# Kernel tuning notes

Hardware: AMD Instinct MI355X
Metric: run time of the kernel (lower is better)

Reference implementation:

```python
import jax, jax.numpy as jnp
import numpy as np

V, D, L, H, SLOTS, FF = 32000, 1024, 6, 16, 4096, 4096
DH = D // H

def rmsnorm(x, w, eps=1e-8):
    return x * jax.lax.rsqrt(jnp.mean(x * x, axis=-1, keepdims=True) + eps) * w

def rope(x):
    # x: [B,T,D]; interleaved RoPE over full d_model as in RoPEEmbedding
    T = x.shape[1]
    inv_freq = 1.0 / (10000.0 ** (jnp.arange(0, D, 2, dtype=jnp.float32) / D))
    freqs = jnp.arange(T, dtype=jnp.float32)[:, None] * inv_freq[None, :]  # [T, D/2]
    cos, sin = jnp.cos(freqs), jnp.sin(freqs)
    x1, x2 = x[..., ::2], x[..., 1::2]
    out = jnp.stack([x1 * cos - x2 * sin, x1 * sin + x2 * cos], axis=-1)
    return out.reshape(x.shape)

def block(x, Wq, Wk, Wv, Wo, bo, n1, Wg, Wu, Wd, n2):
    B, T, _ = x.shape
    q = (x @ Wq).reshape(B, T, H, DH)
    k = (x @ Wk).reshape(B, T, H, DH)
    v = (x @ Wv).reshape(B, T, H, DH)
    scores = jnp.einsum('bqhd,bkhd->bhqk', q, k) * (DH ** -0.5)
    attn = jax.nn.softmax(scores, axis=-1)
    o = jnp.einsum('bhqk,bkhd->bqhd', attn, v).reshape(B, T, D)
    x = rmsnorm(x + o @ Wo + bo, n1)
    ff = (jax.nn.silu(x @ Wg) * (x @ Wu)) @ Wd
    return rmsnorm(x + ff, n2)

def setup_inputs() -> dict:
    key = jax.random.key(0)
    ks = jax.random.split(key, 20)
    nrm = lambda k, s: (jax.random.normal(k, s, jnp.float32) * 0.02)
    inp = {
        'ids': jax.random.randint(ks[0], (2, 2048), 0, V),
        'tok_embed': nrm(ks[1], (V, D)),
        'Wq': nrm(ks[2], (L, D, D)), 'Wk': nrm(ks[3], (L, D, D)),
        'Wv': nrm(ks[4], (L, D, D)), 'Wo': nrm(ks[5], (L, D, D)),
        'bo': jnp.zeros((L, D), jnp.float32),
        'n1': jnp.ones((L, D), jnp.float32),
        'Wg': nrm(ks[6], (L, D, FF)), 'Wu': nrm(ks[7], (L, D, FF)),
        'Wd': nrm(ks[8], (L, FF, D)),
        'n2': jnp.ones((L, D), jnp.float32),
        'mem': nrm(ks[9], (SLOTS, D)),
        'Wsp': nrm(ks[10], (D, D)), 'bsp': jnp.zeros((D,), jnp.float32),
        'Wrp': nrm(ks[11], (D, D)), 'brp': jnp.zeros((D,), jnp.float32),
        'nout': jnp.ones((D,), jnp.float32),
    }
    return inp

def reference(ids, tok_embed, Wq, Wk, Wv, Wo, bo, n1, Wg, Wu, Wd, n2,
              mem, Wsp, bsp, Wrp, brp, nout):
    x = tok_embed[ids]            # [B,T,D] gather
    x = rope(x)
    for i in range(L):
        x = block(x, Wq[i], Wk[i], Wv[i], Wo[i], bo[i], n1[i],
                  Wg[i], Wu[i], Wd[i], n2[i])
    # StateBank content-addressed read: route queries over memory slots
    q = x @ Wsp + bsp                                   # [B,T,D]
    slot_scores = jnp.einsum('btd,sd->bts', q, mem) * (D ** -0.5)
    attention_maps = jax.nn.softmax(slot_scores, axis=-1)  # [B,T,SLOTS]
    r = jnp.einsum('bts,sd->btd', attention_maps, mem)     # gather-route read
    r = r @ Wrp + brp
    h = rmsnorm(x + r, nout)
    logits = h @ tok_embed.T      # tied lm_head
    return logits
```

## Files before the change

### kernel.cpp

```cpp
#include <hip/hip_runtime.h>

typedef __bf16 bf16;
typedef __attribute__((ext_vector_type(8))) __bf16 bf16x8;
typedef __attribute__((ext_vector_type(4))) __bf16 bf16x4;
typedef __attribute__((ext_vector_type(4))) float f32x4;

#define NL 6
#define DIM 1024
#define NH 16
#define DH 64
#define TT 2048
#define BB 2
#define BT 4096
#define FFD 4096
#define NSLOT 4096
#define NV 32000

__device__ __forceinline__ void gld16(const void* g, void* l) {
  __builtin_amdgcn_global_load_lds(
      (const __attribute__((address_space(1))) void*)g,
      (__attribute__((address_space(3))) void*)l, 16, 0, 0);
}


__global__ void cvt_bf16(const float* __restrict__ s, bf16* __restrict__ d, long n) {
  long i = ((long)blockIdx.x * 256 + threadIdx.x) * 4;
  if (i + 3 < n) {
    float4 v = *(const float4*)(s + i);
    bf16x4 o = {(bf16)v.x, (bf16)v.y, (bf16)v.z, (bf16)v.w};
    *(bf16x4*)(d + i) = o;
  }
}

__global__ void transpose_cvt(const float* __restrict__ src, bf16* __restrict__ dst, int R, int C) {
  __shared__ float tile[32][33];
  int c0 = blockIdx.x * 32, r0 = blockIdx.y * 32;
  int tx = threadIdx.x, ty = threadIdx.y;
#pragma unroll
  for (int i = 0; i < 4; ++i)
    tile[ty + i * 8][tx] = src[(size_t)(r0 + ty + i * 8) * C + c0 + tx];
  __syncthreads();
#pragma unroll
  for (int i = 0; i < 4; ++i)
    dst[(size_t)(c0 + ty + i * 8) * R + r0 + tx] = (bf16)tile[tx][ty + i * 8];
}

__global__ void transpose_v(const bf16* __restrict__ v, int ldv, bf16* __restrict__ vT) {
  __shared__ bf16 tile[32][33];
  int t0 = blockIdx.x * 32, d0 = blockIdx.y * 32, bh = blockIdx.z;
  int b = bh >> 4, h = bh & 15;
  int tx = threadIdx.x, ty = threadIdx.y;
#pragma unroll
  for (int i = 0; i < 4; ++i)
    tile[ty + i * 8][tx] = v[(size_t)(b * TT + t0 + ty + i * 8) * ldv + h * DH + d0 + tx];
  __syncthreads();
#pragma unroll
  for (int i = 0; i < 4; ++i)
    vT[((size_t)bh * DH + d0 + ty + i * 8) * TT + t0 + tx] = tile[tx][ty + i * 8];
}


__global__ void embed_rope(const int* __restrict__ ids, const float* __restrict__ emb,
                           float* __restrict__ xf, bf16* __restrict__ xb) {
  int bt = blockIdx.x;
  int t = bt & (TT - 1);
  int id = ids[bt];
  const float* row = emb + (size_t)id * DIM;
  for (int p = threadIdx.x; p < DIM / 2; p += 256) {
    float x1 = row[2 * p], x2 = row[2 * p + 1];
    float inv = __expf(-9.210340371976184f * (float)p * (1.0f / 512.0f));
    float ang = (float)t * inv;
    float c = cosf(ang), s = sinf(ang);
    float o1 = x1 * c - x2 * s;
    float o2 = x1 * s + x2 * c;
    size_t base = (size_t)bt * DIM + 2 * p;
    xf[base] = o1; xf[base + 1] = o2;
    xb[base] = (bf16)o1; xb[base + 1] = (bf16)o2;
  }
}

enum { EP_BF16 = 0, EP_F32 = 1, EP_F32_BIAS = 2, EP_BF16_BIAS = 3, EP_SILU_MUL = 4 };


template <int EP>
__global__ __launch_bounds__(512, 1) void gemm8(
    const bf16* __restrict__ A, const bf16* __restrict__ Bt, void* __restrict__ Cp,
    const float* __restrict__ bias, const bf16* __restrict__ aux,
    int M, int N, int K) {
  __shared__ bf16 S[4][2][256 * 32];

  const int tid = threadIdx.x;
  const int lane = tid & 63;
  const int r16 = lane & 15, hi = lane >> 4;
  const int wave = tid >> 6;
  const int wm = wave >> 2, wn = wave & 3;

  const int nwg = gridDim.x;
  const int orig = blockIdx.x;
  const int qq = nwg >> 3, rr = nwg & 7;
  const int xcd = orig & 7, cidx = orig >> 3;
  const int wg = (xcd < rr ? xcd * (qq + 1) : rr * (qq + 1) + (xcd - rr) * qq) + cidx;
  const int gM = M / 256;
  const int m0 = (wg % gM) * 256;
  const int n0 = (wg / gM) * 256;

  const int srow = tid >> 2;
  const int ccol = tid & 3;
  const int skey = (srow >> 1) & 3;
  const int gcol = (ccol ^ skey) * 8;
  const bf16* aS = A + (size_t)(m0 + srow) * K + gcol;
  const bf16* bS = Bt + (size_t)(n0 + srow) * K + gcol;
  const int dst0 = tid * 8;

  const int rkey = (r16 >> 1) & 3;
  const int rchunk = (hi ^ rkey) * 8;

  f32x4 acc[8][4] = {};
  const int NT = K / 32;

#pragma unroll
  for (int s = 0; s < 3; ++s) {
    gld16(aS + s * 32, &S[s][0][dst0]);
    gld16(aS + s * 32 + (size_t)128 * K, &S[s][0][dst0 + 4096]);
    gld16(bS + s * 32, &S[s][1][dst0]);
    gld16(bS + s * 32 + (size_t)128 * K, &S[s][1][dst0 + 4096]);
  }
  asm volatile("s_waitcnt vmcnt(8)" ::: "memory");
  __builtin_amdgcn_s_barrier();
  __builtin_amdgcn_sched_barrier(0);

  for (int s = 0; s < NT; ++s) {
    const int cs = s & 3, ps = (s + 3) & 3;
    const bool pre = (s + 3) < NT;
    const bf16* SA = S[cs][0];
    const bf16* SB = S[cs][1];
    const size_t koff = (size_t)(s + 3) * 32;
    bf16x8 af[4], bfr[4];

#pragma unroll
    for (int j = 0; j < 4; ++j)
      bfr[j] = *(const bf16x8*)&SB[(wn * 64 + j * 16 + r16) * 32 + rchunk];
#pragma unroll
    for (int i = 0; i < 4; ++i)
      af[i] = *(const bf16x8*)&SA[(wm * 128 + i * 16 + r16) * 32 + rchunk];
    if (pre) {
      gld16(aS + koff, &S[ps][0][dst0]);
      gld16(aS + koff + (size_t)128 * K, &S[ps][0][dst0 + 4096]);
    }
    __builtin_amdgcn_s_barrier();
    __builtin_amdgcn_sched_barrier(0);
    __builtin_amdgcn_s_setprio(1);
#pragma unroll
    for (int i = 0; i < 4; ++i)
#pragma unroll
      for (int j = 0; j < 4; ++j)
        acc[i][j] = __builtin_amdgcn_mfma_f32_16x16x32_bf16(af[i], bfr[j], acc[i][j], 0, 0, 0);
    __builtin_amdgcn_s_setprio(0);
    __builtin_amdgcn_s_barrier();
    __builtin_amdgcn_sched_barrier(0);

#pragma unroll
    for (int i = 0; i < 4; ++i)
      af[i] = *(const bf16x8*)&SA[(wm * 128 + 64 + i * 16 + r16) * 32 + rchunk];
    if (pre) {
      gld16(bS + koff, &S[ps][1][dst0]);
      gld16(bS + koff + (size_t)128 * K, &S[ps][1][dst0 + 4096]);
    }
    __builtin_amdgcn_s_barrier();
    __builtin_amdgcn_sched_barrier(0);
    __builtin_amdgcn_s_setprio(1);
#pragma unroll
    for (int i = 0; i < 4; ++i)
#pragma unroll
      for (int j = 0; j < 4; ++j)
        acc[4 + i][j] = __builtin_amdgcn_mfma_f32_16x16x32_bf16(af[i], bfr[j], acc[4 + i][j], 0, 0, 0);
    __builtin_amdgcn_s_setprio(0);
    if (pre)               asm volatile("s_waitcnt vmcnt(8)" ::: "memory");
    else if ((s + 2) < NT) asm volatile("s_waitcnt vmcnt(4)" ::: "memory");
    else if ((s + 1) < NT) asm volatile("s_waitcnt vmcnt(0)" ::: "memory");
    __builtin_amdgcn_s_barrier();
    __builtin_amdgcn_sched_barrier(0);
  }

#pragma unroll
  for (int mi = 0; mi < 8; ++mi) {
    const int m = m0 + wm * 128 + mi * 16 + hi * 4;
#pragma unroll
    for (int j = 0; j < 4; ++j) {
      const int n = n0 + wn * 64 + j * 16 + r16;
#pragma unroll
      for (int q = 0; q < 4; ++q) {
        size_t idx = (size_t)(m + q) * N + n;
        float v = acc[mi][j][q];
        if constexpr (EP == EP_F32) {
          ((float*)Cp)[idx] = v;
        } else if constexpr (EP == EP_F32_BIAS) {
          ((float*)Cp)[idx] = v + bias[n];
        } else if constexpr (EP == EP_BF16) {
          ((bf16*)Cp)[idx] = (bf16)v;
        } else if constexpr (EP == EP_BF16_BIAS) {
          ((bf16*)Cp)[idx] = (bf16)(v + bias[n]);
        } else {
          float sg = v / (1.0f + __expf(-v));
          ((bf16*)Cp)[idx] = (bf16)(sg * (float)aux[idx]);
        }
      }
    }
  }
}


template <int BM, int BN, int WMW, int WNW, int EP>
__global__ __launch_bounds__(WMW * WNW * 64, 2) void gemmk(
    const bf16* __restrict__ A, const bf16* __restrict__ Bt, void* __restrict__ Cp,
    const float* __restrict__ bias, const bf16* __restrict__ aux,
    int M, int N, int K) {
  constexpr int BK = 32;
  constexpr int NWAVE = WMW * WNW;
  constexpr int NTHR = NWAVE * 64;
  constexpr int MF = BM / (WMW * 16);
  constexpr int NF = BN / (WNW * 16);
  constexpr int AE = BM * BK;
  constexpr int BE = BN * BK;
  constexpr int RHALF = NTHR / 4;
  __shared__ bf16 sA[4][AE];
  __shared__ bf16 sB[4][BE];

  const int tid = threadIdx.x;
  const int lane = tid & 63;
  const int r16 = lane & 15, hi = lane >> 4;
  const int wave = tid >> 6;
  const int wm = wave / WNW, wn = wave % WNW;

  const int nwg = gridDim.x;
  const int orig = blockIdx.x;
  const int qq = nwg >> 3, rr = nwg & 7;
  const int xcd = orig & 7, cidx = orig >> 3;
  const int wg = (xcd < rr ? xcd * (qq + 1) : rr * (qq + 1) + (xcd - rr) * qq) + cidx;
  const int gM = M / BM;
  const int m0 = (wg % gM) * BM;
  const int n0 = (wg / gM) * BN;

  const int srow = tid >> 2;
  const int ccol = tid & 3;
  const int skey = (srow >> 1) & 3;
  const int gcol = ((ccol ^ skey)) * 8;
  const bf16* aS = A + (size_t)(m0 + srow) * K + gcol;
  const bf16* bS = Bt + (size_t)(n0 + srow) * K + gcol;
  const int dst0 = srow * BK + ccol * 8;

  const int rkey = (r16 >> 1) & 3;
  const int rchunk = (hi ^ rkey) * 8;

  f32x4 acc[MF][NF] = {};
  const int NT = K / BK;

  gld16(aS, &sA[0][dst0]);
  gld16(aS + (size_t)RHALF * K, &sA[0][dst0 + RHALF * BK]);
  gld16(bS, &sB[0][dst0]);
  gld16(bS + (size_t)RHALF * K, &sB[0][dst0 + RHALF * BK]);
  gld16(aS + BK, &sA[1][dst0]);
  gld16(aS + BK + (size_t)RHALF * K, &sA[1][dst0 + RHALF * BK]);
  gld16(bS + BK, &sB[1][dst0]);
  gld16(bS + BK + (size_t)RHALF * K, &sB[1][dst0 + RHALF * BK]);

  for (int t = 0; t < NT; ++t) {
    const int cb = t & 3;
    const int pb = (t + 2) & 3;
    const bool pre = (t + 2) < NT;
    if (pre) {
      gld16(aS + (size_t)(t + 2) * BK, &sA[pb][dst0]);
      gld16(aS + (size_t)(t + 2) * BK + (size_t)RHALF * K, &sA[pb][dst0 + RHALF * BK]);
    }
    if (pre)             asm volatile("s_waitcnt vmcnt(6)" ::: "memory");
    else if (t + 1 < NT) asm volatile("s_waitcnt vmcnt(4)" ::: "memory");
    else                 asm volatile("s_waitcnt vmcnt(0)" ::: "memory");
    __builtin_amdgcn_s_barrier();
    __builtin_amdgcn_sched_barrier(0);

    bf16x8 bf_[NF];
#pragma unroll
    for (int j = 0; j < NF; ++j)
      bf_[j] = *(const bf16x8*)&sB[cb][(wn * (NF * 16) + j * 16 + r16) * BK + rchunk];
    if (pre) {
      gld16(bS + (size_t)(t + 2) * BK, &sB[pb][dst0]);
      gld16(bS + (size_t)(t + 2) * BK + (size_t)RHALF * K, &sB[pb][dst0 + RHALF * BK]);
    }
    bf16x8 af[MF];
#pragma unroll
    for (int i = 0; i < MF; ++i)
      af[i] = *(const bf16x8*)&sA[cb][(wm * (MF * 16) + i * 16 + r16) * BK + rchunk];
    __builtin_amdgcn_s_setprio(1);
#pragma unroll
    for (int i = 0; i < MF; ++i)
#pragma unroll
      for (int j = 0; j < NF; ++j)
        acc[i][j] = __builtin_amdgcn_mfma_f32_16x16x32_bf16(af[i], bf_[j], acc[i][j], 0, 0, 0);
    __builtin_amdgcn_s_setprio(0);
  }

#pragma unroll
  for (int i = 0; i < MF; ++i) {
    const int m = m0 + wm * (MF * 16) + i * 16 + hi * 4;
#pragma unroll
    for (int j = 0; j < NF; ++j) {
      const int n = n0 + wn * (NF * 16) + j * 16 + r16;
#pragma unroll
      for (int q = 0; q < 4; ++q) {
        size_t idx = (size_t)(m + q) * N + n;
        float v = acc[i][j][q];
        if constexpr (EP == EP_F32) {
          ((float*)Cp)[idx] = v;
        } else if constexpr (EP == EP_F32_BIAS) {
          ((float*)Cp)[idx] = v + bias[n];
        } else if constexpr (EP == EP_BF16) {
          ((bf16*)Cp)[idx] = (bf16)v;
        } else if constexpr (EP == EP_BF16_BIAS) {
          ((bf16*)Cp)[idx] = (bf16)(v + bias[n]);
        } else {
          float sg = v / (1.0f + __expf(-v));
          ((bf16*)Cp)[idx] = (bf16)(sg * (float)aux[idx]);
        }
      }
    }
  }
}


__global__ __launch_bounds__(256, 2) void attn_flash(
    const bf16* __restrict__ Qp, const bf16* __restrict__ Kp, int ldk,
    const bf16* __restrict__ Vt, bf16* __restrict__ Op) {
  __shared__ bf16 Ks[2][128 * 32];
  __shared__ bf16 Vs[4][64 * 32];
  __shared__ bf16 Ps[4][4][16 * 40];
  const int tid = threadIdx.x, lane = tid & 63, wave = tid >> 6;
  const int h = blockIdx.y, b = blockIdx.z;
  const int r16 = lane & 15, hi = lane >> 4;
  const int qrow = blockIdx.x * 64 + wave * 16 + r16;

  bf16x8 qa[2];
  {
    const bf16* qp = Qp + (size_t)(b * TT + qrow) * ldk + h * DH + hi * 8;
    qa[0] = *(const bf16x8*)qp;
    qa[1] = *(const bf16x8*)(qp + 32);
  }
  const bf16* kBase = Kp + (size_t)(b * TT) * ldk + h * DH;
  const bf16* vBase = Vt + (size_t)(b * NH + h) * DH * TT;

  const int srow = tid >> 2, ccol = tid & 3;
  const int skey = (srow >> 1) & 3;
  const int scolS = (ccol ^ skey) * 8;
  const int dstc = ccol * 8;
  const int rkey = (r16 >> 1) & 3;
  const int rchunk = (hi ^ rkey) * 8;

  float m_run[4] = {-1e30f, -1e30f, -1e30f, -1e30f};
  float l_run[4] = {0.f, 0.f, 0.f, 0.f};
  f32x4 oacc[4] = {};

  for (int kt = 0; kt < TT; kt += 128) {
#pragma unroll
    for (int half = 0; half < 2; ++half) {
      gld16(kBase + (size_t)(kt + srow) * ldk + half * 32 + scolS, &Ks[half][srow * 32 + dstc]);
      gld16(kBase + (size_t)(kt + 64 + srow) * ldk + half * 32 + scolS, &Ks[half][(64 + srow) * 32 + dstc]);
    }
#pragma unroll
    for (int ks = 0; ks < 4; ++ks)
      gld16(vBase + (size_t)srow * TT + kt + ks * 32 + scolS, &Vs[ks][srow * 32 + dstc]);
    __syncthreads();

    f32x4 s[8];
#pragma unroll
    for (int kg = 0; kg < 8; ++kg) {
      f32x4 z = {};
      bf16x8 kb0 = *(const bf16x8*)&Ks[0][(kg * 16 + r16) * 32 + rchunk];
      bf16x8 kb1 = *(const bf16x8*)&Ks[1][(kg * 16 + r16) * 32 + rchunk];
      z = __builtin_amdgcn_mfma_f32_16x16x32_bf16(qa[0], kb0, z, 0, 0, 0);
      z = __builtin_amdgcn_mfma_f32_16x16x32_bf16(qa[1], kb1, z, 0, 0, 0);
      s[kg] = z * 0.125f;
    }
#pragma unroll
    for (int i = 0; i < 4; ++i) {
      float pm = s[0][i];
#pragma unroll
      for (int kg = 1; kg < 8; ++kg) pm = fmaxf(pm, s[kg][i]);
      pm = fmaxf(pm, __shfl_xor(pm, 1));
      pm = fmaxf(pm, __shfl_xor(pm, 2));
      pm = fmaxf(pm, __shfl_xor(pm, 4));
      pm = fmaxf(pm, __shfl_xor(pm, 8));
      float mnew = fmaxf(m_run[i], pm);
      float sc = __expf(m_run[i] - mnew);
      m_run[i] = mnew;
      l_run[i] *= sc;
#pragma unroll
      for (int n = 0; n < 4; ++n) oacc[n][i] *= sc;
#pragma unroll
      for (int kg = 0; kg < 8; ++kg) {
        float p = __expf(s[kg][i] - mnew);
        l_run[i] += p;
        Ps[wave][kg >> 1][(hi * 4 + i) * 40 + (kg & 1) * 16 + r16] = (bf16)p;
      }
    }
#pragma unroll
    for (int ks = 0; ks < 4; ++ks) {
      bf16x8 pa = *(const bf16x8*)&Ps[wave][ks][r16 * 40 + hi * 8];
#pragma unroll
      for (int n = 0; n < 4; ++n) {
        bf16x8 vb = *(const bf16x8*)&Vs[ks][(n * 16 + r16) * 32 + rchunk];
        oacc[n] = __builtin_amdgcn_mfma_f32_16x16x32_bf16(pa, vb, oacc[n], 0, 0, 0);
      }
    }
    __syncthreads();
  }

#pragma unroll
  for (int i = 0; i < 4; ++i) {
    float l = l_run[i];
    l += __shfl_xor(l, 1);
    l += __shfl_xor(l, 2);
    l += __shfl_xor(l, 4);
    l += __shfl_xor(l, 8);
    float inv = 1.0f / l;
    int trow = blockIdx.x * 64 + wave * 16 + hi * 4 + i;
    size_t base = ((size_t)b * TT + trow) * DIM + h * DH;
#pragma unroll
    for (int n = 0; n < 4; ++n)
      Op[base + n * 16 + r16] = (bf16)(oacc[n][i] * inv);
  }
}


__global__ __launch_bounds__(256) void resid_rms(
    const float* __restrict__ xin, const float* __restrict__ y, const float* __restrict__ wgt,
    float* __restrict__ xf_out, bf16* __restrict__ xb_out) {
  __shared__ float red[4];
  const int r = blockIdx.x, tid = threadIdx.x;
  const size_t base = (size_t)r * DIM + tid * 4;
  float4 v = *(const float4*)(xin + base);
  float4 u = *(const float4*)(y + base);
  v.x += u.x; v.y += u.y; v.z += u.z; v.w += u.w;
  float ss = v.x * v.x + v.y * v.y + v.z * v.z + v.w * v.w;
#pragma unroll
  for (int d = 1; d < 64; d <<= 1) ss += __shfl_xor(ss, d);
  if ((tid & 63) == 0) red[tid >> 6] = ss;
  __syncthreads();
  ss = red[0] + red[1] + red[2] + red[3];
  float sc = rsqrtf(ss * (1.0f / DIM) + 1e-8f);
  const float4 wv = *(const float4*)(wgt + tid * 4);
  float o0 = v.x * sc * wv.x, o1 = v.y * sc * wv.y, o2 = v.z * sc * wv.z, o3 = v.w * sc * wv.w;
  if (xf_out) {
    float4 ov = {o0, o1, o2, o3};
    *(float4*)(xf_out + base) = ov;
  }
  bf16x4 ob = {(bf16)o0, (bf16)o1, (bf16)o2, (bf16)o3};
  *(bf16x4*)(xb_out + base) = ob;
}


__global__ __launch_bounds__(256) void softmax_rows(const float* __restrict__ Sc, bf16* __restrict__ P) {
  __shared__ float red[4];
  const int r = blockIdx.x, tid = threadIdx.x;
  const float* row = Sc + (size_t)r * NSLOT;
  float4 v[4];
#pragma unroll
  for (int i = 0; i < 4; ++i) v[i] = *(const float4*)(row + tid * 4 + i * 1024);
  float mx = -1e30f;
#pragma unroll
  for (int i = 0; i < 4; ++i)
    mx = fmaxf(fmaxf(fmaxf(fmaxf(mx, v[i].x), v[i].y), v[i].z), v[i].w);
#pragma unroll
  for (int d = 1; d < 64; d <<= 1) mx = fmaxf(mx, __shfl_xor(mx, d));
  if ((tid & 63) == 0) red[tid >> 6] = mx;
  __syncthreads();
  mx = fmaxf(fmaxf(red[0], red[1]), fmaxf(red[2], red[3]));
  __syncthreads();
  float e[16];
  float sum = 0.f;
#pragma unroll
  for (int i = 0; i < 4; ++i) {
    e[i * 4 + 0] = __expf((v[i].x - mx) * 0.03125f);
    e[i * 4 + 1] = __expf((v[i].y - mx) * 0.03125f);
    e[i * 4 + 2] = __expf((v[i].z - mx) * 0.03125f);
    e[i * 4 + 3] = __expf((v[i].w - mx) * 0.03125f);
    sum += e[i * 4 + 0] + e[i * 4 + 1] + e[i * 4 + 2] + e[i * 4 + 3];
  }
#pragma unroll
  for (int d = 1; d < 64; d <<= 1) sum += __shfl_xor(sum, d);
  if ((tid & 63) == 0) red[tid >> 6] = sum;
  __syncthreads();
  sum = red[0] + red[1] + red[2] + red[3];
  float inv = 1.0f / sum;
#pragma unroll
  for (int i = 0; i < 4; ++i) {
    bf16x4 ob = {(bf16)(e[i * 4 + 0] * inv), (bf16)(e[i * 4 + 1] * inv),
                 (bf16)(e[i * 4 + 2] * inv), (bf16)(e[i * 4 + 3] * inv)};
    *(bf16x4*)(P + (size_t)r * NSLOT + tid * 4 + i * 1024) = ob;
  }
}


extern "C" void kernel_launch(void* const* d_in, const int* in_sizes, int n_in,
                              void* d_out, int out_size, void* d_ws, size_t ws_size,
                              hipStream_t stream) {
  (void)in_sizes; (void)n_in; (void)out_size;
  const int* ids = (const int*)d_in[0];
  const float* emb = (const float*)d_in[1];
  const float* Wq = (const float*)d_in[2];
  const float* Wk = (const float*)d_in[3];
  const float* Wv = (const float*)d_in[4];
  const float* Wo = (const float*)d_in[5];
  const float* bo = (const float*)d_in[6];
  const float* n1 = (const float*)d_in[7];
  const float* Wg = (const float*)d_in[8];
  const float* Wu = (const float*)d_in[9];
  const float* Wd = (const float*)d_in[10];
  const float* n2 = (const float*)d_in[11];
  const float* memp = (const float*)d_in[12];
  const float* Wsp = (const float*)d_in[13];
  const float* bsp = (const float*)d_in[14];
  const float* Wrp = (const float*)d_in[15];
  const float* brp = (const float*)d_in[16];
  const float* nout = (const float*)d_in[17];

  char* w = (char*)d_ws;
  auto alloc = [&](size_t bytes) -> void* {
    void* p = (void*)w;
    w += (bytes + 255) & ~(size_t)255;
    return p;
  };

  const size_t dd = (size_t)DIM * DIM;
  const size_t dff = (size_t)DIM * FFD;

  bf16* tok_b = (bf16*)alloc((size_t)NV * DIM * 2);
  bf16* mem_b = (bf16*)alloc((size_t)NSLOT * DIM * 2);
  bf16* memT  = (bf16*)alloc((size_t)NSLOT * DIM * 2);
  bf16* WspT  = (bf16*)alloc(dd * 2);
  bf16* WrpT  = (bf16*)alloc(dd * 2);
  float* xf   = (float*)alloc((size_t)BT * DIM * 4);
  bf16* xb    = (bf16*)alloc((size_t)BT * DIM * 2);
  float* yb   = (float*)alloc((size_t)BT * DIM * 4);
  bf16* W3T   = (bf16*)alloc(3 * dd * 2);
  bf16* WoT   = (bf16*)alloc(dd * 2);
  bf16* WgT   = (bf16*)alloc(dff * 2);
  bf16* WuT   = (bf16*)alloc(dff * 2);
  bf16* WdT   = (bf16*)alloc(dff * 2);
  bf16* qkv   = (bf16*)alloc((size_t)BT * 3 * DIM * 2);
  bf16* vT_   = (bf16*)alloc((size_t)BT * DIM * 2);
  bf16* ot_   = (bf16*)alloc((size_t)BT * DIM * 2);
  bf16* qb    = (bf16*)alloc((size_t)BT * DIM * 2);
  bf16* rb    = (bf16*)alloc((size_t)BT * DIM * 2);
  bf16* hb    = (bf16*)alloc((size_t)BT * DIM * 2);

  size_t used = (size_t)(w - (char*)d_ws);
  size_t region_bytes = (size_t)BT * NSLOT * 4 + (size_t)BT * NSLOT * 2;
  char* region;
  if (used + region_bytes <= ws_size) region = (char*)alloc(region_bytes);
  else region = (char*)d_out;
  bf16* Ub = (bf16*)region;
  bf16* Hb = (bf16*)(region + (size_t)BT * FFD * 2);
  float* scoresF = (float*)region;
  bf16* attnb = (bf16*)(region + (size_t)BT * NSLOT * 4);

  dim3 blkT(32, 8);

  cvt_bf16<<<NV * DIM / 1024, 256, 0, stream>>>(emb, tok_b, (long)NV * DIM);
  cvt_bf16<<<NSLOT * DIM / 1024, 256, 0, stream>>>(memp, mem_b, (long)NSLOT * DIM);
  transpose_cvt<<<dim3(DIM / 32, NSLOT / 32), blkT, 0, stream>>>(memp, memT, NSLOT, DIM);
  transpose_cvt<<<dim3(DIM / 32, DIM / 32), blkT, 0, stream>>>(Wsp, WspT, DIM, DIM);
  transpose_cvt<<<dim3(DIM / 32, DIM / 32), blkT, 0, stream>>>(Wrp, WrpT, DIM, DIM);
  embed_rope<<<BT, 256, 0, stream>>>(ids, emb, xf, xb);

  for (int l = 0; l < NL; ++l) {
    transpose_cvt<<<dim3(32, 32), blkT, 0, stream>>>(Wq + l * dd, W3T, DIM, DIM);
    transpose_cvt<<<dim3(32, 32), blkT, 0, stream>>>(Wk + l * dd, W3T + dd, DIM, DIM);
    transpose_cvt<<<dim3(32, 32), blkT, 0, stream>>>(Wv + l * dd, W3T + 2 * dd, DIM, DIM);
    transpose_cvt<<<dim3(32, 32), blkT, 0, stream>>>(Wo + l * dd, WoT, DIM, DIM);
    transpose_cvt<<<dim3(FFD / 32, DIM / 32), blkT, 0, stream>>>(Wg + l * dff, WgT, DIM, FFD);
    transpose_cvt<<<dim3(FFD / 32, DIM / 32), blkT, 0, stream>>>(Wu + l * dff, WuT, DIM, FFD);
    transpose_cvt<<<dim3(DIM / 32, FFD / 32), blkT, 0, stream>>>(Wd + l * dff, WdT, FFD, DIM);

    gemm8<EP_BF16><<<dim3(16 * 12), 512, 0, stream>>>(
        xb, W3T, qkv, nullptr, nullptr, BT, 3 * DIM, DIM);
    transpose_v<<<dim3(TT / 32, DH / 32, BB * NH), blkT, 0, stream>>>(qkv + 2 * DIM, 3 * DIM, vT_);
    attn_flash<<<dim3(TT / 64, NH, BB), 256, 0, stream>>>(qkv, qkv + DIM, 3 * DIM, vT_, ot_);
    gemmk<128, 128, 2, 2, EP_F32_BIAS><<<dim3(8 * 32), 256, 0, stream>>>(
        ot_, WoT, yb, bo + l * DIM, nullptr, BT, DIM, DIM);
    resid_rms<<<BT, 256, 0, stream>>>(xf, yb, n1 + l * DIM, xf, xb);
    gemm8<EP_BF16><<<dim3(16 * 16), 512, 0, stream>>>(
        xb, WuT, Ub, nullptr, nullptr, BT, FFD, DIM);
    gemm8<EP_SILU_MUL><<<dim3(16 * 16), 512, 0, stream>>>(
        xb, WgT, Hb, nullptr, Ub, BT, FFD, DIM);
    gemmk<128, 128, 2, 2, EP_F32><<<dim3(8 * 32), 256, 0, stream>>>(
        Hb, WdT, yb, nullptr, nullptr, BT, DIM, FFD);
    resid_rms<<<BT, 256, 0, stream>>>(xf, yb, n2 + l * DIM, xf, xb);
  }

  gemmk<128, 128, 2, 2, EP_BF16_BIAS><<<dim3(8 * 32), 256, 0, stream>>>(
      xb, WspT, qb, bsp, nullptr, BT, DIM, DIM);
  gemm8<EP_F32><<<dim3(16 * 16), 512, 0, stream>>>(
      qb, mem_b, scoresF, nullptr, nullptr, BT, NSLOT, DIM);
  softmax_rows<<<BT, 256, 0, stream>>>(scoresF, attnb);
  gemmk<128, 128, 2, 2, EP_BF16><<<dim3(8 * 32), 256, 0, stream>>>(
      attnb, memT, rb, nullptr, nullptr, BT, DIM, NSLOT);
  gemmk<128, 128, 2, 2, EP_F32_BIAS><<<dim3(8 * 32), 256, 0, stream>>>(
      rb, WrpT, yb, brp, nullptr, BT, DIM, DIM);
  resid_rms<<<BT, 256, 0, stream>>>(xf, yb, nout, nullptr, hb);
  gemm8<EP_F32><<<dim3(16 * 125), 512, 0, stream>>>(
      hb, tok_b, (float*)d_out, nullptr, nullptr, BT, NV, DIM);
}
```

Measured before the change: 2.924 ms.

## Vectorize weight transpose, shrink flash-attention key tile, use gemmk for QKV

The weight transpose kernel now loads a float4 per thread and stores bf16x4, using a new 8x32 block shape, while the V transpose keeps the old shape. The flash attention kernel processes 64 keys per iteration instead of 128, which roughly halves shared memory and register use, and its launch bounds ask for 4 blocks per CU. The QKV projection switches from gemm8 with 512 threads to the gemmk 128x128 tile kernel with a larger grid. Smaller attention tiles mean twice as many barriers and loop iterations, and the QKV kernel swap may change GEMM efficiency.

```diff
diff --git a/kernel.cpp b/kernel.cpp
--- a/kernel.cpp
+++ b/kernel.cpp
@@ -35,14 +35,17 @@
 __global__ void transpose_cvt(const float* __restrict__ src, bf16* __restrict__ dst, int R, int C) {
   __shared__ float tile[32][33];
   int c0 = blockIdx.x * 32, r0 = blockIdx.y * 32;
-  int tx = threadIdx.x, ty = threadIdx.y;
-#pragma unroll
-  for (int i = 0; i < 4; ++i)
-    tile[ty + i * 8][tx] = src[(size_t)(r0 + ty + i * 8) * C + c0 + tx];
+  int tx = threadIdx.x;
+  int ty = threadIdx.y;
+  float4 v = *(const float4*)(src + (size_t)(r0 + ty) * C + c0 + tx * 4);
+  tile[ty][tx * 4 + 0] = v.x;
+  tile[ty][tx * 4 + 1] = v.y;
+  tile[ty][tx * 4 + 2] = v.z;
+  tile[ty][tx * 4 + 3] = v.w;
   __syncthreads();
-#pragma unroll
-  for (int i = 0; i < 4; ++i)
-    dst[(size_t)(c0 + ty + i * 8) * R + r0 + tx] = (bf16)tile[tx][ty + i * 8];
+  bf16x4 o = {(bf16)tile[tx * 4 + 0][ty], (bf16)tile[tx * 4 + 1][ty],
+              (bf16)tile[tx * 4 + 2][ty], (bf16)tile[tx * 4 + 3][ty]};
+  *(bf16x4*)(dst + (size_t)(c0 + ty) * R + r0 + tx * 4) = o;
 }
 
 __global__ void transpose_v(const bf16* __restrict__ v, int ldv, bf16* __restrict__ vT) {
@@ -327,12 +330,12 @@
 }
 
 
-__global__ __launch_bounds__(256, 2) void attn_flash(
+__global__ __launch_bounds__(256, 4) void attn_flash(
     const bf16* __restrict__ Qp, const bf16* __restrict__ Kp, int ldk,
     const bf16* __restrict__ Vt, bf16* __restrict__ Op) {
-  __shared__ bf16 Ks[2][128 * 32];
-  __shared__ bf16 Vs[4][64 * 32];
-  __shared__ bf16 Ps[4][4][16 * 40];
+  __shared__ bf16 Ks[2][64 * 32];
+  __shared__ bf16 Vs[2][64 * 32];
+  __shared__ bf16 Ps[4][2][16 * 40];
   const int tid = threadIdx.x, lane = tid & 63, wave = tid >> 6;
   const int h = blockIdx.y, b = blockIdx.z;
   const int r16 = lane & 15, hi = lane >> 4;
@@ -358,20 +361,18 @@
   float l_run[4] = {0.f, 0.f, 0.f, 0.f};
   f32x4 oacc[4] = {};
 
-  for (int kt = 0; kt < TT; kt += 128) {
-#pragma unroll
-    for (int half = 0; half < 2; ++half) {
+  for (int kt = 0; kt < TT; kt += 64) {
+#pragma unroll
+    for (int half = 0; half < 2; ++half)
       gld16(kBase + (size_t)(kt + srow) * ldk + half * 32 + scolS, &Ks[half][srow * 32 + dstc]);
-      gld16(kBase + (size_t)(kt + 64 + srow) * ldk + half * 32 + scolS, &Ks[half][(64 + srow) * 32 + dstc]);
-    }
-#pragma unroll
-    for (int ks = 0; ks < 4; ++ks)
+#pragma unroll
+    for (int ks = 0; ks < 2; ++ks)
       gld16(vBase + (size_t)srow * TT + kt + ks * 32 + scolS, &Vs[ks][srow * 32 + dstc]);
     __syncthreads();
 
-    f32x4 s[8];
-#pragma unroll
-    for (int kg = 0; kg < 8; ++kg) {
+    f32x4 s[4];
+#pragma unroll
+    for (int kg = 0; kg < 4; ++kg) {
       f32x4 z = {};
       bf16x8 kb0 = *(const bf16x8*)&Ks[0][(kg * 16 + r16) * 32 + rchunk];
       bf16x8 kb1 = *(const bf16x8*)&Ks[1][(kg * 16 + r16) * 32 + rchunk];
@@ -381,9 +382,7 @@
     }
 #pragma unroll
     for (int i = 0; i < 4; ++i) {
-      float pm = s[0][i];
-#pragma unroll
-      for (int kg = 1; kg < 8; ++kg) pm = fmaxf(pm, s[kg][i]);
+      float pm = fmaxf(fmaxf(s[0][i], s[1][i]), fmaxf(s[2][i], s[3][i]));
       pm = fmaxf(pm, __shfl_xor(pm, 1));
       pm = fmaxf(pm, __shfl_xor(pm, 2));
       pm = fmaxf(pm, __shfl_xor(pm, 4));
@@ -395,14 +394,14 @@
 #pragma unroll
       for (int n = 0; n < 4; ++n) oacc[n][i] *= sc;
 #pragma unroll
-      for (int kg = 0; kg < 8; ++kg) {
+      for (int kg = 0; kg < 4; ++kg) {
         float p = __expf(s[kg][i] - mnew);
         l_run[i] += p;
         Ps[wave][kg >> 1][(hi * 4 + i) * 40 + (kg & 1) * 16 + r16] = (bf16)p;
       }
     }
 #pragma unroll
-    for (int ks = 0; ks < 4; ++ks) {
+    for (int ks = 0; ks < 2; ++ks) {
       bf16x8 pa = *(const bf16x8*)&Ps[wave][ks][r16 * 40 + hi * 8];
 #pragma unroll
       for (int n = 0; n < 4; ++n) {
@@ -562,7 +561,8 @@
   float* scoresF = (float*)region;
   bf16* attnb = (bf16*)(region + (size_t)BT * NSLOT * 4);
 
-  dim3 blkT(32, 8);
+  dim3 blkT(8, 32);
+  dim3 blkV(32, 8);
 
   cvt_bf16<<<NV * DIM / 1024, 256, 0, stream>>>(emb, tok_b, (long)NV * DIM);
   cvt_bf16<<<NSLOT * DIM / 1024, 256, 0, stream>>>(memp, mem_b, (long)NSLOT * DIM);
@@ -580,9 +580,9 @@
     transpose_cvt<<<dim3(FFD / 32, DIM / 32), blkT, 0, stream>>>(Wu + l * dff, WuT, DIM, FFD);
     transpose_cvt<<<dim3(DIM / 32, FFD / 32), blkT, 0, stream>>>(Wd + l * dff, WdT, FFD, DIM);
 
-    gemm8<EP_BF16><<<dim3(16 * 12), 512, 0, stream>>>(
+    gemmk<128, 128, 2, 2, EP_BF16><<<dim3(32 * 24), 256, 0, stream>>>(
         xb, W3T, qkv, nullptr, nullptr, BT, 3 * DIM, DIM);
-    transpose_v<<<dim3(TT / 32, DH / 32, BB * NH), blkT, 0, stream>>>(qkv + 2 * DIM, 3 * DIM, vT_);
+    transpose_v<<<dim3(TT / 32, DH / 32, BB * NH), blkV, 0, stream>>>(qkv + 2 * DIM, 3 * DIM, vT_);
     attn_flash<<<dim3(TT / 64, NH, BB), 256, 0, stream>>>(qkv, qkv + DIM, 3 * DIM, vT_, ot_);
     gemmk<128, 128, 2, 2, EP_F32_BIAS><<<dim3(8 * 32), 256, 0, stream>>>(
         ot_, WoT, yb, bo + l * DIM, nullptr, BT, DIM, DIM);
```

Result: slower. 3.037 ms (+3.9%).
